# Optimization experiments

Measured on AMD Instinct MI355X. Metric: run time of the kernel, lower is better.

## Reference

```python
import jax, jax.numpy as jnp
import numpy as np

SEQ, SUB, B, V = 32, 16, 512, 258
U = SEQ // SUB
Z, CH, CO, DH = 512, 1024, 512, 1024


def _lstm_cell(x, h, c, Wi, Wh, bi, bh):
    # torch gate order: input, forget, cell, output
    g = x @ Wi + h @ Wh + bi + bh  # [B, 4H]
    i, f, gg, o = jnp.split(g, 4, axis=-1)
    c = jax.nn.sigmoid(f) * c + jax.nn.sigmoid(i) * jnp.tanh(gg)
    h = jax.nn.sigmoid(o) * jnp.tanh(c)
    return h, c


def _lstm2(xs, h1_0, p1, p2):
    # xs: [T,B,in]; h1_0: [B,H] layer-1 initial hidden.
    # Layer-2 hidden and both cell states start at zero (initialize_state in torch code).
    z0 = jnp.zeros_like(h1_0)
    def step(carry, x):
        h1, c1, h2, c2 = carry
        h1, c1 = _lstm_cell(x, h1, c1, *p1)
        h2, c2 = _lstm_cell(h1, h2, c2, *p2)
        return (h1, c1, h2, c2), h2
    _, hs = jax.lax.scan(step, (h1_0, z0, z0, z0), xs)
    return hs  # [T,B,H] top-layer hidden states


def setup_inputs() -> dict:
    key = jax.random.key(0)
    ks = iter(jax.random.split(key, 40))
    def w(shape, s=0.05):
        return jax.random.normal(next(ks), shape, dtype=jnp.float32) * s
    return {
        "z": jax.random.normal(next(ks), (B, Z), dtype=jnp.float32),
        "x": jax.random.uniform(next(ks), (SEQ, B, V), dtype=jnp.float32),
        "conductor_input": w((1, B, V)),
        "ci_W": w((Z, CH)), "ci_b": w((CH,)),
        "cW1i": w((V, 4 * CH)), "cW1h": w((CH, 4 * CH)), "cb1i": w((4 * CH,)), "cb1h": w((4 * CH,)),
        "cW2i": w((CH, 4 * CH)), "cW2h": w((CH, 4 * CH)), "cb2i": w((4 * CH,)), "cb2h": w((4 * CH,)),
        "co_W": w((CH, CO)), "co_b": w((CO,)),
        "di_W": w((CO, DH)), "di_b": w((DH,)),
        "dW1i": w((CO + V, 4 * DH)), "dW1h": w((DH, 4 * DH)), "db1i": w((4 * DH,)), "db1h": w((4 * DH,)),
        "dW2i": w((DH, 4 * DH)), "dW2h": w((DH, 4 * DH)), "db2i": w((4 * DH,)), "db2h": w((4 * DH,)),
        "fc_W": w((DH, V)), "fc_b": w((V,)),
    }


def reference(z, x, conductor_input, ci_W, ci_b, cW1i, cW1h, cb1i, cb1h, cW2i, cW2h, cb2i, cb2h, co_W, co_b, di_W, di_b, dW1i, dW1h, db1i, db1h, dW2i, dW2h, db2i, db2h, fc_W, fc_b):
    # --- conductor: 2-layer LSTM over U steps of a learned constant input ---
    h1 = jnp.tanh(z @ ci_W + ci_b)  # [B,CH] layer-1 init hidden
    cin = jnp.broadcast_to(conductor_input, (U, B, V))
    ch = _lstm2(cin, h1, (cW1i, cW1h, cb1i, cb1h), (cW2i, cW2h, cb2i, cb2h))  # [U,B,CH]
    c = ch @ co_W + co_b  # [U,B,CO]
    # --- decoder (teacher forcing): state resets each sub-sequence, so the U
    # segments of length SUB are independent given c -> vmap over segments ---
    sos = jnp.zeros((1, B, V), jnp.float32).at[:, :, 0].set(1.0)
    prev = jnp.concatenate([sos, x[:-1]], axis=0).reshape(U, SUB, B, V)
    cb = jnp.broadcast_to(c[:, None], (U, SUB, B, CO))
    dec_in = jnp.concatenate([cb, prev], axis=-1)  # [U,SUB,B,CO+V]
    def run_seg(xs, cj):
        h1_0 = jnp.tanh(cj @ di_W + di_b)  # [B,DH]
        return _lstm2(xs, h1_0, (dW1i, dW1h, db1i, db1h), (dW2i, dW2h, db2i, db2h))
    hs = jax.vmap(run_seg)(dec_in, c)  # [U,SUB,B,DH]
    logp = jax.nn.log_softmax(hs @ fc_W + fc_b, axis=-1)  # log(softmax(.)) fused
    return logp.reshape(SEQ, B, V).transpose(1, 0, 2)  # [B,SEQ,V]
```

## Files before the change

kernel.cpp:

```cpp
#include <hip/hip_runtime.h>
#include <cstddef>
#include <cstdint>


namespace {

typedef short s8v __attribute__((ext_vector_type(8)));
typedef float f4v __attribute__((ext_vector_type(4)));
typedef unsigned short ushort_t;

__device__ inline unsigned short f2bf(float f) {
    union { float f; unsigned u; } v; v.f = f;
    unsigned r = v.u + 0x7fff + ((v.u >> 16) & 1);
    return (unsigned short)(r >> 16);
}
__device__ inline float bf2f(ushort_t u) {
    union { unsigned u; float f; } v; v.u = ((unsigned)u) << 16; return v.f;
}
__device__ inline float sigm_f(float x) { return 1.f / (1.f + __expf(-x)); }
__device__ inline float tanh_f(float x) {
    const float e = __expf(2.f * fabsf(x));
    return copysignf(1.f - 2.f / (e + 1.f), x);
}

#define GLOAD_LDS(gp, lp)                                              \
    __builtin_amdgcn_global_load_lds(                                  \
        (const __attribute__((address_space(1))) void*)(gp),           \
        (__attribute__((address_space(3))) void*)(lp), 16, 0, 0)

__device__ __forceinline__ void gemm_core(
    const ushort_t* __restrict__ A1a, const ushort_t* __restrict__ A1b,
    int lda1, int K1, const ushort_t* __restrict__ B1t,
    const ushort_t* __restrict__ A2, int lda2, int K2,
    const ushort_t* __restrict__ B2t,
    int bm, int bn, ushort_t* lds, f4v acc[4][4])
{
    const int tid = threadIdx.x;
    const int wid = tid >> 6;
    const int lane = tid & 63;

    const int sr0 = wid * 16 + (lane >> 2);
    const int sr1 = sr0 + 64;
    const int rl0 = sr0 ^ ((sr0 >> 2) & 1);
    const int rl1 = sr1 ^ ((sr1 >> 2) & 1);
    const int c0 = (((lane & 3) ^ (rl0 & 3)) << 3);
    const int c1 = (((lane & 3) ^ (rl1 & 3)) << 3);
    const int ldst = wid * 512;

    auto arow = [&](const ushort_t* Aa, const ushort_t* Ab, int lda,
                    int r) -> const ushort_t* {
        return (Ab != nullptr && r >= 512) ? Ab + (size_t)(r - 512) * lda
                                           : Aa + (size_t)r * lda;
    };
    const ushort_t* a1r0 = arow(A1a, A1b, lda1, bm + rl0) + c0;
    const ushort_t* a1r1 = arow(A1a, A1b, lda1, bm + rl1) + c1;
    const ushort_t* b1r0 = B1t + (size_t)(bn + rl0) * K1 + c0;
    const ushort_t* b1r1 = B1t + (size_t)(bn + rl1) * K1 + c1;
    const int n1 = K1 >> 5, n2 = (B2t != nullptr) ? (K2 >> 5) : 0;
    const int nt = n1 + n2;
    const ushort_t* a2r0 = nullptr; const ushort_t* a2r1 = nullptr;
    const ushort_t* b2r0 = nullptr; const ushort_t* b2r1 = nullptr;
    if (n2 > 0) {
        a2r0 = A2 + (size_t)(bm + rl0) * lda2 + c0;
        a2r1 = A2 + (size_t)(bm + rl1) * lda2 + c1;
        b2r0 = B2t + (size_t)(bn + rl0) * K2 + c0;
        b2r1 = B2t + (size_t)(bn + rl1) * K2 + c1;
    }

    auto stage = [&](int idx, int buf) {
        ushort_t* Lb = lds + buf * 8192;
        const ushort_t *pa0, *pa1, *pb0, *pb1;
        if (idx < n1) {
            const int k0 = idx << 5;
            pa0 = a1r0 + k0; pa1 = a1r1 + k0; pb0 = b1r0 + k0; pb1 = b1r1 + k0;
        } else {
            const int k0 = (idx - n1) << 5;
            pa0 = a2r0 + k0; pa1 = a2r1 + k0; pb0 = b2r0 + k0; pb1 = b2r1 + k0;
        }
        GLOAD_LDS(pa0, Lb + ldst);
        GLOAD_LDS(pa1, Lb + 2048 + ldst);
        GLOAD_LDS(pb0, Lb + 4096 + ldst);
        GLOAD_LDS(pb1, Lb + 6144 + ldst);
    };

    const int wr = wid >> 1, wc = wid & 1;
    const int lrow = lane & 15, lkg = lane >> 4;
    int aoff[4], boff[4];
#pragma unroll
    for (int m = 0; m < 4; ++m) {
        const int r = wr * 64 + m * 16 + lrow;
        aoff[m] = (r ^ ((r >> 2) & 1)) * 32 + ((lkg ^ (r & 3)) << 3);
    }
#pragma unroll
    for (int n = 0; n < 4; ++n) {
        const int r = wc * 64 + n * 16 + lrow;
        boff[n] = 4096 + (r ^ ((r >> 2) & 1)) * 32 + ((lkg ^ (r & 3)) << 3);
    }

    stage(0, 0);
    stage(1, 1);
    int sbuf = 2, cbuf = 0;
    for (int t = 0; t < nt; ++t) {
        if (t == nt - 1) {
            asm volatile("s_waitcnt vmcnt(0)" ::: "memory");
        } else {
            asm volatile("s_waitcnt vmcnt(4)" ::: "memory");
        }
        __builtin_amdgcn_s_barrier();
        __builtin_amdgcn_sched_barrier(0);
        if (t + 2 < nt) {
            stage(t + 2, sbuf);
            sbuf = (sbuf == 2) ? 0 : sbuf + 1;
        }
        const ushort_t* L = lds + cbuf * 8192;
        s8v af[4], bv[4];
#pragma unroll
        for (int m = 0; m < 4; ++m) af[m] = *(const s8v*)(L + aoff[m]);
#pragma unroll
        for (int n = 0; n < 4; ++n) bv[n] = *(const s8v*)(L + boff[n]);
        __builtin_amdgcn_s_setprio(1);
#pragma unroll
        for (int m = 0; m < 4; ++m)
#pragma unroll
            for (int n = 0; n < 4; ++n)
                acc[m][n] = __builtin_amdgcn_mfma_f32_16x16x32_bf16(
                    af[m], bv[n], acc[m][n], 0, 0, 0);
        __builtin_amdgcn_s_setprio(0);
        cbuf = (cbuf == 2) ? 0 : cbuf + 1;
    }
}

template <int ACT>
__global__ __launch_bounds__(256) void plain_gemm(
    const ushort_t* __restrict__ A, int lda, int K,
    const ushort_t* __restrict__ Bt,
    const float* __restrict__ bias, int bias_n,
    float* __restrict__ C, ushort_t* __restrict__ Cbf, int N)
{
    __shared__ __align__(16) ushort_t lds[3 * 8192];
    const int bm = blockIdx.x * 128, bn = blockIdx.y * 128;
    f4v acc[4][4] = {};
    gemm_core(A, nullptr, lda, K, Bt, nullptr, 0, 0, nullptr, bm, bn, lds, acc);

    const int tid = threadIdx.x, wid = tid >> 6, lane = tid & 63;
    const int wr = wid >> 1, wc = wid & 1, lrow = lane & 15, lkg = lane >> 4;
#pragma unroll
    for (int m = 0; m < 4; ++m) {
        const int row0 = bm + wr * 64 + m * 16 + lkg * 4;
#pragma unroll
        for (int n = 0; n < 4; ++n) {
            const int col = bn + wc * 64 + n * 16 + lrow;
            const float bv = (bias != nullptr && col < bias_n) ? bias[col] : 0.f;
#pragma unroll
            for (int r = 0; r < 4; ++r) {
                float v = acc[m][n][r] + bv;
                if (ACT == 1) v = tanh_f(v);
                const size_t o = (size_t)(row0 + r) * N + col;
                if (C != nullptr) C[o] = v;
                if (Cbf != nullptr) Cbf[o] = f2bf(v);
            }
        }
    }
}

struct Prob {
    const ushort_t* A1a; const ushort_t* A1b; int lda1; int K1;
    const ushort_t* B1t;
    const ushort_t* A2; int lda2; int K2; const ushort_t* B2t;
    const ushort_t* Dbf;
    const float* bias;
    float* cst;
    ushort_t* hout;
    ushort_t* hs;
    int step_s;
};

__global__ __launch_bounds__(256) void lstm_step(Prob PA, int nxa, Prob PB,
                                                 int mshift)
{
    __shared__ __align__(16) ushort_t lds[3 * 8192];
    const int nblk = gridDim.x;
    const int wg = blockIdx.x;
    const int swz = (wg & 7) * (nblk >> 3) + (wg >> 3);
    const int nmb = 1 << mshift;
    const int nb = swz >> mshift;
    const int mb = swz & (nmb - 1);

    const bool isA = mb < nxa;
    const Prob& P = isA ? PA : PB;
    const int bm = (isA ? mb : mb - nxa) * 128;
    const int bn = nb * 128;

    f4v acc[4][4] = {};
    gemm_core(P.A1a, P.A1b, P.lda1, P.K1, P.B1t,
              P.A2, P.lda2, P.K2, P.B2t, bm, bn, lds, acc);

    const int tid = threadIdx.x, wid = tid >> 6, lane = tid & 63;
    const int wr = wid >> 1, wc = wid & 1, lrow = lane & 15, lkg = lane >> 4;
    const int colbase = bn + wc * 64;
    const int jb = (colbase >> 6) * 16 + lrow;

#pragma unroll
    for (int m = 0; m < 4; ++m) {
        const int row0 = bm + wr * 64 + m * 16 + lkg * 4;
#pragma unroll
        for (int r = 0; r < 4; ++r) {
            const int row = row0 + r;
            float g0 = acc[m][0][r], g1 = acc[m][1][r];
            float g2 = acc[m][2][r], g3 = acc[m][3][r];
            if (P.Dbf != nullptr) {
                const ushort_t* d = P.Dbf + (size_t)row * 4096 + colbase + lrow;
                g0 += bf2f(d[0]); g1 += bf2f(d[16]);
                g2 += bf2f(d[32]); g3 += bf2f(d[48]);
            }
            if (P.bias != nullptr) {
                const float* b = P.bias + colbase + lrow;
                g0 += b[0]; g1 += b[16]; g2 += b[32]; g3 += b[48];
            }
            const size_t ci = (size_t)row * 1024 + jb;
            const float cn = fmaf(sigm_f(g1), P.cst[ci], sigm_f(g0) * tanh_f(g2));
            const float hn = sigm_f(g3) * tanh_f(cn);
            P.cst[ci] = cn;
            const ushort_t hb = f2bf(hn);
            P.hout[ci] = hb;
            if (P.hs != nullptr) {
                size_t d;
                if (P.step_s >= 0) {
                    const int u = row >> 9, b = row & 511;
                    d = ((size_t)((u * 16 + P.step_s) * 512 + b) << 10) + jb;
                } else {
                    d = ci;
                }
                P.hs[d] = hb;
            }
        }
    }
}

template <int PERM>
__global__ __launch_bounds__(256) void transpose_to_bf16(
    const float* __restrict__ in, ushort_t* __restrict__ out,
    int K, int N, int Kp, int Np)
{
    __shared__ float tile[32][33];
    const int k0 = blockIdx.x * 32, n0 = blockIdx.y * 32;
    const int tx = threadIdx.x, ty = threadIdx.y;
#pragma unroll
    for (int q = 0; q < 4; ++q) {
        const int k = k0 + ty + 8 * q, n = n0 + tx;
        tile[ty + 8 * q][tx] = (k < K && n < N) ? in[(size_t)k * N + n] : 0.f;
    }
    __syncthreads();
#pragma unroll
    for (int q = 0; q < 4; ++q) {
        const int n = n0 + ty + 8 * q, k = k0 + tx;
        int np = n;
        if (PERM) np = ((n & 1023) >> 4) * 64 + (n >> 10) * 16 + (n & 15);
        out[(size_t)np * Kp + k] = f2bf(tile[tx][ty + 8 * q]);
    }
}

__global__ void convert_pad_bf16(const float* __restrict__ in,
                                 ushort_t* __restrict__ out,
                                 int K, int Kp, int total)
{
    const int idx = blockIdx.x * 256 + threadIdx.x;
    if (idx >= total) return;
    const int r = idx / Kp, k = idx - r * Kp;
    out[idx] = (k < K) ? f2bf(in[(size_t)r * K + k]) : (ushort_t)0;
}

__global__ void sos_init_bf16(ushort_t* __restrict__ sos)
{
    const int i = blockIdx.x * 256 + threadIdx.x;
    if (i < 512 * 288) sos[i] = ((i % 288) == 0) ? (ushort_t)0x3F80 : (ushort_t)0;
}

__global__ void permute_bias(const float* __restrict__ b1,
                             const float* __restrict__ b2,
                             float* __restrict__ out)
{
    const int c = blockIdx.x * 256 + threadIdx.x;
    if (c >= 4096) return;
    const int g = (c >> 4) & 3;
    const int j = (c >> 6) * 16 + (c & 15);
    out[c] = b1[g * 1024 + j] + b2[g * 1024 + j];
}

__global__ __launch_bounds__(256) void logsoftmax_kernel(
    const float* __restrict__ logits, float* __restrict__ out)
{
    const int row = blockIdx.x;
    const int tid = threadIdx.x;
    const float* L = logits + (size_t)row * 384;
    const int t = row >> 9;
    const int b = row & 511;
    float* O = out + ((size_t)b * 32 + t) * 258;

    const float x0 = L[tid];
    const float x1 = (tid < 2) ? L[256 + tid] : -1e30f;

    __shared__ float sm[4];
    float m = fmaxf(x0, x1);
#pragma unroll
    for (int off = 32; off > 0; off >>= 1) m = fmaxf(m, __shfl_down(m, off));
    if ((tid & 63) == 0) sm[tid >> 6] = m;
    __syncthreads();
    m = fmaxf(fmaxf(sm[0], sm[1]), fmaxf(sm[2], sm[3]));
    __syncthreads();

    float s = expf(x0 - m) + ((tid < 2) ? expf(x1 - m) : 0.f);
#pragma unroll
    for (int off = 32; off > 0; off >>= 1) s += __shfl_down(s, off);
    if ((tid & 63) == 0) sm[tid >> 6] = s;
    __syncthreads();
    s = sm[0] + sm[1] + sm[2] + sm[3];

    const float lse = m + logf(s);
    O[tid] = x0 - lse;
    if (tid < 2) O[256 + tid] = x1 - lse;
}

}

extern "C" void kernel_launch(void* const* d_in, const int* in_sizes, int n_in,
                              void* d_out, int out_size, void* d_ws, size_t ws_size,
                              hipStream_t stream)
{
    (void)in_sizes; (void)n_in; (void)out_size; (void)ws_size;

    const float* z    = (const float*)d_in[0];
    const float* x    = (const float*)d_in[1];
    const float* cin  = (const float*)d_in[2];
    const float* ciW  = (const float*)d_in[3];
    const float* cib  = (const float*)d_in[4];
    const float* cW1i = (const float*)d_in[5];
    const float* cW1h = (const float*)d_in[6];
    const float* cb1i = (const float*)d_in[7];
    const float* cb1h = (const float*)d_in[8];
    const float* cW2i = (const float*)d_in[9];
    const float* cW2h = (const float*)d_in[10];
    const float* cb2i = (const float*)d_in[11];
    const float* cb2h = (const float*)d_in[12];
    const float* coW  = (const float*)d_in[13];
    const float* cob  = (const float*)d_in[14];
    const float* diW  = (const float*)d_in[15];
    const float* dib  = (const float*)d_in[16];
    const float* dW1i = (const float*)d_in[17];
    const float* dW1h = (const float*)d_in[18];
    const float* db1i = (const float*)d_in[19];
    const float* db1h = (const float*)d_in[20];
    const float* dW2i = (const float*)d_in[21];
    const float* dW2h = (const float*)d_in[22];
    const float* db2i = (const float*)d_in[23];
    const float* db2h = (const float*)d_in[24];
    const float* fcW  = (const float*)d_in[25];
    const float* fcb  = (const float*)d_in[26];
    float* out = (float*)d_out;

    char* wsp = (char*)d_ws;
    size_t off = 0;
    auto allocf = [&](size_t n) { float* p = (float*)(wsp + off); off += n * 4; return p; };
    auto allocb = [&](size_t n) { ushort_t* p = (ushort_t*)(wsp + off); off += n * 2; return p; };

    float* cst = allocf((size_t)3 * 1024 * 1024 + 64);
    float* c1c = cst;
    float* c2c = cst + (size_t)512 * 1024;
    float* c1d = cst + (size_t)1024 * 1024;
    float* c2d = cst + (size_t)2 * 1024 * 1024;
    float* pb1c = allocf(4096);
    float* pb2c = allocf(4096);
    float* pb1d = allocf(4096);
    float* pb2d = allocf(4096);
    float* logits = allocf((size_t)16384 * 384);

    ushort_t* h2z  = allocb((size_t)2 * (512 + 1024) * 1024);
    ushort_t* hc2A = h2z;
    ushort_t* hc2B = h2z + (size_t)512 * 1024;
    ushort_t* h2dA = h2z + (size_t)2 * 512 * 1024;
    ushort_t* h2dB = h2z + (size_t)(2 * 512 + 1024) * 1024;

    ushort_t* hc1A = allocb((size_t)512 * 1024);
    ushort_t* hc1B = allocb((size_t)512 * 1024);
    ushort_t* h1dA = allocb((size_t)1024 * 1024);
    ushort_t* h1dB = allocb((size_t)1024 * 1024);

    ushort_t* zbf    = allocb((size_t)512 * 512);
    ushort_t* cinbf  = allocb((size_t)512 * 288);
    ushort_t* sosbf  = allocb((size_t)512 * 288);
    ushort_t* xbf    = allocb((size_t)16384 * 288);
    ushort_t* chbf   = allocb((size_t)1024 * 1024);
    ushort_t* ccode  = allocb((size_t)1024 * 512);
    ushort_t* cpre   = allocb((size_t)1024 * 4096);
    ushort_t* xW1c   = allocb((size_t)512 * 4096);
    ushort_t* hsbf   = allocb((size_t)16384 * 1024);

    ushort_t* ciWt  = allocb((size_t)1024 * 512);
    ushort_t* cW1it = allocb((size_t)4096 * 288);
    ushort_t* cW1ht = allocb((size_t)4096 * 1024);
    ushort_t* cW2it = allocb((size_t)4096 * 1024);
    ushort_t* cW2ht = allocb((size_t)4096 * 1024);
    ushort_t* coWt  = allocb((size_t)512 * 1024);
    ushort_t* dtopt = allocb((size_t)4096 * 512);
    ushort_t* dbott = allocb((size_t)4096 * 288);
    ushort_t* diWt  = allocb((size_t)1024 * 512);
    ushort_t* dW1ht = allocb((size_t)4096 * 1024);
    ushort_t* dW2it = allocb((size_t)4096 * 1024);
    ushort_t* dW2ht = allocb((size_t)4096 * 1024);
    ushort_t* fcWt  = allocb((size_t)384 * 1024);

    hipMemsetAsync(cst, 0, (size_t)3 * 1024 * 1024 * 4, stream);
    hipMemsetAsync(h2z, 0, (size_t)2 * (512 + 1024) * 1024 * 2, stream);

    auto transp = [&](const float* in, ushort_t* o, int K, int N, int Kp, int Np, int perm) {
        dim3 g(Kp / 32, Np / 32), b(32, 8);
        if (perm) transpose_to_bf16<1><<<g, b, 0, stream>>>(in, o, K, N, Kp, Np);
        else      transpose_to_bf16<0><<<g, b, 0, stream>>>(in, o, K, N, Kp, Np);
    };
    transp(ciW, ciWt, 512, 1024, 512, 1024, 0);
    transp(cW1i, cW1it, 258, 4096, 288, 4096, 1);
    transp(cW1h, cW1ht, 1024, 4096, 1024, 4096, 1);
    transp(cW2i, cW2it, 1024, 4096, 1024, 4096, 1);
    transp(cW2h, cW2ht, 1024, 4096, 1024, 4096, 1);
    transp(coW, coWt, 1024, 512, 1024, 512, 0);
    transp(dW1i, dtopt, 512, 4096, 512, 4096, 1);
    transp(dW1i + (size_t)512 * 4096, dbott, 258, 4096, 288, 4096, 1);
    transp(diW, diWt, 512, 1024, 512, 1024, 0);
    transp(dW1h, dW1ht, 1024, 4096, 1024, 4096, 1);
    transp(dW2i, dW2it, 1024, 4096, 1024, 4096, 1);
    transp(dW2h, dW2ht, 1024, 4096, 1024, 4096, 1);
    transp(fcW, fcWt, 1024, 258, 1024, 384, 0);

    auto convert = [&](const float* in, ushort_t* o, int K, int Kp, int R) {
        const int total = R * Kp;
        convert_pad_bf16<<<dim3((total + 255) / 256), 256, 0, stream>>>(in, o, K, Kp, total);
    };
    convert(z, zbf, 512, 512, 512);
    convert(cin, cinbf, 258, 288, 512);
    convert(x, xbf, 258, 288, 16384);
    sos_init_bf16<<<dim3((512 * 288 + 255) / 256), 256, 0, stream>>>(sosbf);
    permute_bias<<<16, 256, 0, stream>>>(cb1i, cb1h, pb1c);
    permute_bias<<<16, 256, 0, stream>>>(cb2i, cb2h, pb2c);
    permute_bias<<<16, 256, 0, stream>>>(db1i, db1h, pb1d);
    permute_bias<<<16, 256, 0, stream>>>(db2i, db2h, pb2d);

    auto gemm = [&](int act, const ushort_t* A, int lda, int K, const ushort_t* Bt,
                    const float* bias, int bias_n,
                    float* C, ushort_t* Cbf, int M, int N) {
        dim3 g(M / 128, N / 128);
        if (act) plain_gemm<1><<<g, 256, 0, stream>>>(A, lda, K, Bt, bias, bias_n, C, Cbf, N);
        else     plain_gemm<0><<<g, 256, 0, stream>>>(A, lda, K, Bt, bias, bias_n, C, Cbf, N);
    };

    gemm(1, zbf, 512, 512, ciWt, cib, 1024, nullptr, hc1A, 512, 1024);
    gemm(0, cinbf, 288, 288, cW1it, pb1c, 4096, nullptr, xW1c, 512, 4096);

    ushort_t* HC1[2] = {hc1A, hc1B};
    ushort_t* HC2[2] = {hc2A, hc2B};
    for (int k = 0; k <= 2; ++k) {
        Prob pa{}, pb{};
        int nxa = 0, nxb = 0;
        if (k < 2) {
            pa = {HC1[k & 1], nullptr, 1024, 1024, cW1ht,
                  nullptr, 0, 0, nullptr,
                  xW1c, nullptr, c1c, HC1[(k + 1) & 1], nullptr, -1};
            nxa = 4;
        }
        if (k >= 1) {
            pb = {HC1[k & 1], nullptr, 1024, 1024, cW2it,
                  HC2[k & 1], 1024, 1024, cW2ht,
                  nullptr, pb2c, c2c, HC2[(k + 1) & 1],
                  chbf + (size_t)(k - 1) * 512 * 1024, -1};
            nxb = 4;
        }
        const int nmb = nxa + nxb;
        const int mshift = (nmb == 4) ? 2 : 3;
        lstm_step<<<dim3(nmb * 32), 256, 0, stream>>>(pa, nxa, pb, mshift);
    }

    gemm(0, chbf, 1024, 1024, coWt, cob, 512, nullptr, ccode, 1024, 512);
    gemm(0, ccode, 512, 512, dtopt, pb1d, 4096, nullptr, cpre, 1024, 4096);
    gemm(1, ccode, 512, 512, diWt, dib, 1024, nullptr, h1dA, 1024, 1024);

    ushort_t* H1[2] = {h1dA, h1dB};
    ushort_t* H2[2] = {h2dA, h2dB};
    for (int k = 0; k <= 16; ++k) {
        Prob pa{}, pb{};
        int nxa = 0, nxb = 0;
        if (k < 16) {
            const ushort_t* plo = (k == 0) ? sosbf : (xbf + (size_t)(k - 1) * 512 * 288);
            const ushort_t* phi = xbf + (size_t)(15 + k) * 512 * 288;
            pa = {plo, phi, 288, 288, dbott,
                  H1[k & 1], 1024, 1024, dW1ht,
                  cpre, nullptr, c1d, H1[(k + 1) & 1], nullptr, -1};
            nxa = 8;
        }
        if (k >= 1) {
            pb = {H1[k & 1], nullptr, 1024, 1024, dW2it,
                  H2[k & 1], 1024, 1024, dW2ht,
                  nullptr, pb2d, c2d, H2[(k + 1) & 1], hsbf, k - 1};
            nxb = 8;
        }
        const int nmb = nxa + nxb;
        const int mshift = (nmb == 8) ? 3 : 4;
        lstm_step<<<dim3(nmb * 32), 256, 0, stream>>>(pa, nxa, pb, mshift);
    }

    gemm(0, hsbf, 1024, 1024, fcWt, fcb, 258, logits, nullptr, 16384, 384);
    logsoftmax_kernel<<<dim3(16384), 256, 0, stream>>>(logits, out);
}
```

Baseline: 1.108 ms.

## Pre-pack weights into MFMA fragment layout and load B directly to registers

```diff
diff --git a/kernel.cpp b/kernel.cpp
--- a/kernel.cpp
+++ b/kernel.cpp
@@ -30,117 +30,118 @@
 
 __device__ __forceinline__ void gemm_core(
     const ushort_t* __restrict__ A1a, const ushort_t* __restrict__ A1b,
-    int lda1, int K1, const ushort_t* __restrict__ B1t,
+    int lda1, int K1, const ushort_t* __restrict__ W1,
     const ushort_t* __restrict__ A2, int lda2, int K2,
-    const ushort_t* __restrict__ B2t,
+    const ushort_t* __restrict__ W2,
     int bm, int bn, ushort_t* lds, f4v acc[4][4])
 {
     const int tid = threadIdx.x;
     const int wid = tid >> 6;
     const int lane = tid & 63;
-
-    const int sr0 = wid * 16 + (lane >> 2);
-    const int sr1 = sr0 + 64;
-    const int rl0 = sr0 ^ ((sr0 >> 2) & 1);
-    const int rl1 = sr1 ^ ((sr1 >> 2) & 1);
-    const int c0 = (((lane & 3) ^ (rl0 & 3)) << 3);
-    const int c1 = (((lane & 3) ^ (rl1 & 3)) << 3);
-    const int ldst = wid * 512;
+    const int wr = wid >> 1, wc = wid & 1;
+    const int lrow = lane & 15, lkg = lane >> 4;
+
+    const int n1 = K1 >> 5;
+    const int n2 = (W2 != nullptr) ? (K2 >> 5) : 0;
+    const int nt = n1 + n2;
+
+    const int row0 = wid * 16 + (lane >> 2);
+    const int row1 = row0 + 64;
+    const int src0 = (((lane & 3) ^ ((row0 >> 1) & 3)) << 3);
+    const int src1 = (((lane & 3) ^ ((row1 >> 1) & 3)) << 3);
 
     auto arow = [&](const ushort_t* Aa, const ushort_t* Ab, int lda,
                     int r) -> const ushort_t* {
         return (Ab != nullptr && r >= 512) ? Ab + (size_t)(r - 512) * lda
                                            : Aa + (size_t)r * lda;
     };
-    const ushort_t* a1r0 = arow(A1a, A1b, lda1, bm + rl0) + c0;
-    const ushort_t* a1r1 = arow(A1a, A1b, lda1, bm + rl1) + c1;
-    const ushort_t* b1r0 = B1t + (size_t)(bn + rl0) * K1 + c0;
-    const ushort_t* b1r1 = B1t + (size_t)(bn + rl1) * K1 + c1;
-    const int n1 = K1 >> 5, n2 = (B2t != nullptr) ? (K2 >> 5) : 0;
-    const int nt = n1 + n2;
-    const ushort_t* a2r0 = nullptr; const ushort_t* a2r1 = nullptr;
-    const ushort_t* b2r0 = nullptr; const ushort_t* b2r1 = nullptr;
+    const ushort_t* pA1q0 = arow(A1a, A1b, lda1, bm + row0) + src0;
+    const ushort_t* pA1q1 = arow(A1a, A1b, lda1, bm + row1) + src1;
+    const ushort_t* pA2q0 = nullptr;
+    const ushort_t* pA2q1 = nullptr;
     if (n2 > 0) {
-        a2r0 = A2 + (size_t)(bm + rl0) * lda2 + c0;
-        a2r1 = A2 + (size_t)(bm + rl1) * lda2 + c1;
-        b2r0 = B2t + (size_t)(bn + rl0) * K2 + c0;
-        b2r1 = B2t + (size_t)(bn + rl1) * K2 + c1;
-    }
-
-    auto stage = [&](int idx, int buf) {
-        ushort_t* Lb = lds + buf * 8192;
-        const ushort_t *pa0, *pa1, *pb0, *pb1;
-        if (idx < n1) {
-            const int k0 = idx << 5;
-            pa0 = a1r0 + k0; pa1 = a1r1 + k0; pb0 = b1r0 + k0; pb1 = b1r1 + k0;
-        } else {
-            const int k0 = (idx - n1) << 5;
-            pa0 = a2r0 + k0; pa1 = a2r1 + k0; pb0 = b2r0 + k0; pb1 = b2r1 + k0;
-        }
-        GLOAD_LDS(pa0, Lb + ldst);
-        GLOAD_LDS(pa1, Lb + 2048 + ldst);
-        GLOAD_LDS(pb0, Lb + 4096 + ldst);
-        GLOAD_LDS(pb1, Lb + 6144 + ldst);
-    };
-
-    const int wr = wid >> 1, wc = wid & 1;
-    const int lrow = lane & 15, lkg = lane >> 4;
-    int aoff[4], boff[4];
+        pA2q0 = A2 + (size_t)(bm + row0) * lda2 + src0;
+        pA2q1 = A2 + (size_t)(bm + row1) * lda2 + src1;
+    }
+
+    int sbuf = 2;
+    auto stageA = [&](int idx, int buf) {
+        const ushort_t *p0, *p1;
+        if (idx < n1) { p0 = pA1q0 + (idx << 5); p1 = pA1q1 + (idx << 5); }
+        else { const int i2 = idx - n1; p0 = pA2q0 + (i2 << 5); p1 = pA2q1 + (i2 << 5); }
+        GLOAD_LDS(p0, lds + buf * 4096 + wid * 512);
+        GLOAD_LDS(p1, lds + buf * 4096 + 2048 + wid * 512);
+    };
+
+    const int nb0 = (bn >> 4) + wc * 4;
+    const ushort_t* W1l = W1 + (size_t)nb0 * n1 * 512 + lane * 8;
+    const ushort_t* W2l = (n2 > 0) ? (W2 + (size_t)nb0 * n2 * 512 + lane * 8) : nullptr;
+
+    auto loadB = [&](int t, s8v (&b)[4]) {
+        const ushort_t* base; int kb, KB;
+        if (t < n1) { base = W1l; kb = t; KB = n1; }
+        else        { base = W2l; kb = t - n1; KB = n2; }
+#pragma unroll
+        for (int n = 0; n < 4; ++n)
+            b[n] = *(const s8v*)(base + ((size_t)(n * KB + kb) << 9));
+    };
+
+    int aoff[4];
 #pragma unroll
     for (int m = 0; m < 4; ++m) {
         const int r = wr * 64 + m * 16 + lrow;
-        aoff[m] = (r ^ ((r >> 2) & 1)) * 32 + ((lkg ^ (r & 3)) << 3);
-    }
-#pragma unroll
-    for (int n = 0; n < 4; ++n) {
-        const int r = wc * 64 + n * 16 + lrow;
-        boff[n] = 4096 + (r ^ ((r >> 2) & 1)) * 32 + ((lkg ^ (r & 3)) << 3);
-    }
-
-    stage(0, 0);
-    stage(1, 1);
-    int sbuf = 2, cbuf = 0;
-    for (int t = 0; t < nt; ++t) {
-        if (t == nt - 1) {
-            asm volatile("s_waitcnt vmcnt(0)" ::: "memory");
-        } else {
-            asm volatile("s_waitcnt vmcnt(4)" ::: "memory");
-        }
+        aoff[m] = r * 32 + ((lkg ^ ((r >> 1) & 3)) << 3);
+    }
+
+    s8v bA[4], bB[4];
+    loadB(0, bA);
+    stageA(0, 0);
+    if (nt > 1) stageA(1, 1);
+
+    int cbuf = 0;
+    auto iter = [&](int t, s8v (&bcur)[4], s8v (&bnxt)[4]) {
+        if (t + 1 < nt) loadB(t + 1, bnxt);
+        if (t + 1 < nt) asm volatile("s_waitcnt vmcnt(6)" ::: "memory");
+        else            asm volatile("s_waitcnt vmcnt(0)" ::: "memory");
         __builtin_amdgcn_s_barrier();
         __builtin_amdgcn_sched_barrier(0);
         if (t + 2 < nt) {
-            stage(t + 2, sbuf);
+            stageA(t + 2, sbuf);
             sbuf = (sbuf == 2) ? 0 : sbuf + 1;
         }
-        const ushort_t* L = lds + cbuf * 8192;
-        s8v af[4], bv[4];
-#pragma unroll
-        for (int m = 0; m < 4; ++m) af[m] = *(const s8v*)(L + aoff[m]);
-#pragma unroll
-        for (int n = 0; n < 4; ++n) bv[n] = *(const s8v*)(L + boff[n]);
+        const ushort_t* L = lds + cbuf * 4096;
+        s8v a[4];
+#pragma unroll
+        for (int m = 0; m < 4; ++m) a[m] = *(const s8v*)(L + aoff[m]);
         __builtin_amdgcn_s_setprio(1);
 #pragma unroll
         for (int m = 0; m < 4; ++m)
 #pragma unroll
             for (int n = 0; n < 4; ++n)
                 acc[m][n] = __builtin_amdgcn_mfma_f32_16x16x32_bf16(
-                    af[m], bv[n], acc[m][n], 0, 0, 0);
+                    a[m], bcur[n], acc[m][n], 0, 0, 0);
         __builtin_amdgcn_s_setprio(0);
         cbuf = (cbuf == 2) ? 0 : cbuf + 1;
+    };
+
+    int t = 0;
+    while (true) {
+        iter(t, bA, bB); if (++t == nt) break;
+        iter(t, bB, bA); if (++t == nt) break;
     }
 }
 
 template <int ACT>
-__global__ __launch_bounds__(256) void plain_gemm(
+__global__ __launch_bounds__(256, 2) void plain_gemm(
     const ushort_t* __restrict__ A, int lda, int K,
-    const ushort_t* __restrict__ Bt,
+    const ushort_t* __restrict__ W,
     const float* __restrict__ bias, int bias_n,
     float* __restrict__ C, ushort_t* __restrict__ Cbf, int N)
 {
-    __shared__ __align__(16) ushort_t lds[3 * 8192];
+    __shared__ __align__(16) ushort_t lds[3 * 4096];
     const int bm = blockIdx.x * 128, bn = blockIdx.y * 128;
     f4v acc[4][4] = {};
-    gemm_core(A, nullptr, lda, K, Bt, nullptr, 0, 0, nullptr, bm, bn, lds, acc);
+    gemm_core(A, nullptr, lda, K, W, nullptr, 0, 0, nullptr, bm, bn, lds, acc);
 
     const int tid = threadIdx.x, wid = tid >> 6, lane = tid & 63;
     const int wr = wid >> 1, wc = wid & 1, lrow = lane & 15, lkg = lane >> 4;
@@ -175,10 +176,10 @@
     int step_s;
 };
 
-__global__ __launch_bounds__(256) void lstm_step(Prob PA, int nxa, Prob PB,
-                                                 int mshift)
-{
-    __shared__ __align__(16) ushort_t lds[3 * 8192];
+__global__ __launch_bounds__(256, 2) void lstm_step(Prob PA, int nxa, Prob PB,
+                                                    int mshift)
+{
+    __shared__ __align__(16) ushort_t lds[3 * 4096];
     const int nblk = gridDim.x;
     const int wg = blockIdx.x;
     const int swz = (wg & 7) * (nblk >> 3) + (wg >> 3);
@@ -238,26 +239,39 @@
 }
 
 template <int PERM>
-__global__ __launch_bounds__(256) void transpose_to_bf16(
+__global__ __launch_bounds__(256) void pack_frag_bf16(
     const float* __restrict__ in, ushort_t* __restrict__ out,
     int K, int N, int Kp, int Np)
 {
     __shared__ float tile[32][33];
-    const int k0 = blockIdx.x * 32, n0 = blockIdx.y * 32;
-    const int tx = threadIdx.x, ty = threadIdx.y;
+    const int kb = blockIdx.x;
+    const int np0 = blockIdx.y * 32;
+    const int k0 = kb * 32;
+    const int tx = threadIdx.x & 31;
+    const int ty = threadIdx.x >> 5;
 #pragma unroll
     for (int q = 0; q < 4; ++q) {
-        const int k = k0 + ty + 8 * q, n = n0 + tx;
+        const int k = k0 + ty + 8 * q;
+        const int np = np0 + tx;
+        int n;
+        if (PERM) n = ((np >> 4) & 3) * 1024 + (np >> 6) * 16 + (np & 15);
+        else      n = np;
         tile[ty + 8 * q][tx] = (k < K && n < N) ? in[(size_t)k * N + n] : 0.f;
     }
     __syncthreads();
-#pragma unroll
-    for (int q = 0; q < 4; ++q) {
-        const int n = n0 + ty + 8 * q, k = k0 + tx;
-        int np = n;
-        if (PERM) np = ((n & 1023) >> 4) * 64 + (n >> 10) * 16 + (n & 15);
-        out[(size_t)np * Kp + k] = f2bf(tile[tx][ty + 8 * q]);
-    }
+    const int t = threadIdx.x;
+    const int rec = t >> 7;
+    const int lane = (t >> 1) & 63;
+    const int half = t & 1;
+    const size_t grec = (size_t)(np0 / 16 + rec) * (Kp / 32) + kb;
+    const int kl = (lane >> 4) * 8 + half * 4;
+    const int nl = rec * 16 + (lane & 15);
+    ushort4 v;
+    v.x = f2bf(tile[kl + 0][nl]);
+    v.y = f2bf(tile[kl + 1][nl]);
+    v.z = f2bf(tile[kl + 2][nl]);
+    v.w = f2bf(tile[kl + 3][nl]);
+    *(ushort4*)(out + (grec * 64 + lane) * 8 + half * 4) = v;
 }
 
 __global__ void convert_pad_bf16(const float* __restrict__ in,
@@ -273,7 +287,7 @@
 __global__ void sos_init_bf16(ushort_t* __restrict__ sos)
 {
     const int i = blockIdx.x * 256 + threadIdx.x;
-    if (i < 512 * 288) sos[i] = ((i % 288) == 0) ? (ushort_t)0x3F80 : (ushort_t)0;
+    if (i < 512 * 320) sos[i] = ((i % 320) == 0) ? (ushort_t)0x3F80 : (ushort_t)0;
 }
 
 __global__ void permute_bias(const float* __restrict__ b1,
@@ -386,74 +400,74 @@
     ushort_t* h1dB = allocb((size_t)1024 * 1024);
 
     ushort_t* zbf    = allocb((size_t)512 * 512);
-    ushort_t* cinbf  = allocb((size_t)512 * 288);
-    ushort_t* sosbf  = allocb((size_t)512 * 288);
-    ushort_t* xbf    = allocb((size_t)16384 * 288);
+    ushort_t* cinbf  = allocb((size_t)512 * 320);
+    ushort_t* sosbf  = allocb((size_t)512 * 320);
+    ushort_t* xbf    = allocb((size_t)16384 * 320);
     ushort_t* chbf   = allocb((size_t)1024 * 1024);
     ushort_t* ccode  = allocb((size_t)1024 * 512);
     ushort_t* cpre   = allocb((size_t)1024 * 4096);
     ushort_t* xW1c   = allocb((size_t)512 * 4096);
     ushort_t* hsbf   = allocb((size_t)16384 * 1024);
 
-    ushort_t* ciWt  = allocb((size_t)1024 * 512);
-    ushort_t* cW1it = allocb((size_t)4096 * 288);
-    ushort_t* cW1ht = allocb((size_t)4096 * 1024);
-    ushort_t* cW2it = allocb((size_t)4096 * 1024);
-    ushort_t* cW2ht = allocb((size_t)4096 * 1024);
-    ushort_t* coWt  = allocb((size_t)512 * 1024);
-    ushort_t* dtopt = allocb((size_t)4096 * 512);
-    ushort_t* dbott = allocb((size_t)4096 * 288);
-    ushort_t* diWt  = allocb((size_t)1024 * 512);
-    ushort_t* dW1ht = allocb((size_t)4096 * 1024);
-    ushort_t* dW2it = allocb((size_t)4096 * 1024);
-    ushort_t* dW2ht = allocb((size_t)4096 * 1024);
-    ushort_t* fcWt  = allocb((size_t)384 * 1024);
+    ushort_t* ciWp  = allocb((size_t)1024 * 512);
+    ushort_t* cW1ip = allocb((size_t)4096 * 320);
+    ushort_t* cW1hp = allocb((size_t)4096 * 1024);
+    ushort_t* cW2ip = allocb((size_t)4096 * 1024);
+    ushort_t* cW2hp = allocb((size_t)4096 * 1024);
+    ushort_t* coWp  = allocb((size_t)512 * 1024);
+    ushort_t* dtopp = allocb((size_t)4096 * 512);
+    ushort_t* dbotp = allocb((size_t)4096 * 320);
+    ushort_t* diWp  = allocb((size_t)1024 * 512);
+    ushort_t* dW1hp = allocb((size_t)4096 * 1024);
+    ushort_t* dW2ip = allocb((size_t)4096 * 1024);
+    ushort_t* dW2hp = allocb((size_t)4096 * 1024);
+    ushort_t* fcWp  = allocb((size_t)384 * 1024);
 
     hipMemsetAsync(cst, 0, (size_t)3 * 1024 * 1024 * 4, stream);
     hipMemsetAsync(h2z, 0, (size_t)2 * (512 + 1024) * 1024 * 2, stream);
 
-    auto transp = [&](const float* in, ushort_t* o, int K, int N, int Kp, int Np, int perm) {
-        dim3 g(Kp / 32, Np / 32), b(32, 8);
-        if (perm) transpose_to_bf16<1><<<g, b, 0, stream>>>(in, o, K, N, Kp, Np);
-        else      transpose_to_bf16<0><<<g, b, 0, stream>>>(in, o, K, N, Kp, Np);
-    };
-    transp(ciW, ciWt, 512, 1024, 512, 1024, 0);
-    transp(cW1i, cW1it, 258, 4096, 288, 4096, 1);
-    transp(cW1h, cW1ht, 1024, 4096, 1024, 4096, 1);
-    transp(cW2i, cW2it, 1024, 4096, 1024, 4096, 1);
-    transp(cW2h, cW2ht, 1024, 4096, 1024, 4096, 1);
-    transp(coW, coWt, 1024, 512, 1024, 512, 0);
-    transp(dW1i, dtopt, 512, 4096, 512, 4096, 1);
-    transp(dW1i + (size_t)512 * 4096, dbott, 258, 4096, 288, 4096, 1);
-    transp(diW, diWt, 512, 1024, 512, 1024, 0);
-    transp(dW1h, dW1ht, 1024, 4096, 1024, 4096, 1);
-    transp(dW2i, dW2it, 1024, 4096, 1024, 4096, 1);
-    transp(dW2h, dW2ht, 1024, 4096, 1024, 4096, 1);
-    transp(fcW, fcWt, 1024, 258, 1024, 384, 0);
+    auto pack = [&](const float* in, ushort_t* o, int K, int N, int Kp, int Np, int perm) {
+        dim3 g(Kp / 32, Np / 32);
+        if (perm) pack_frag_bf16<1><<<g, 256, 0, stream>>>(in, o, K, N, Kp, Np);
+        else      pack_frag_bf16<0><<<g, 256, 0, stream>>>(in, o, K, N, Kp, Np);
+    };
+    pack(ciW, ciWp, 512, 1024, 512, 1024, 0);
+    pack(cW1i, cW1ip, 258, 4096, 320, 4096, 1);
+    pack(cW1h, cW1hp, 1024, 4096, 1024, 4096, 1);
+    pack(cW2i, cW2ip, 1024, 4096, 1024, 4096, 1);
+    pack(cW2h, cW2hp, 1024, 4096, 1024, 4096, 1);
+    pack(coW, coWp, 1024, 512, 1024, 512, 0);
+    pack(dW1i, dtopp, 512, 4096, 512, 4096, 1);
+    pack(dW1i + (size_t)512 * 4096, dbotp, 258, 4096, 320, 4096, 1);
+    pack(diW, diWp, 512, 1024, 512, 1024, 0);
+    pack(dW1h, dW1hp, 1024, 4096, 1024, 4096, 1);
+    pack(dW2i, dW2ip, 1024, 4096, 1024, 4096, 1);
+    pack(dW2h, dW2hp, 1024, 4096, 1024, 4096, 1);
+    pack(fcW, fcWp, 1024, 258, 1024, 384, 0);
 
     auto convert = [&](const float* in, ushort_t* o, int K, int Kp, int R) {
         const int total = R * Kp;
         convert_pad_bf16<<<dim3((total + 255) / 256), 256, 0, stream>>>(in, o, K, Kp, total);
     };
     convert(z, zbf, 512, 512, 512);
-    convert(cin, cinbf, 258, 288, 512);
-    convert(x, xbf, 258, 288, 16384);
-    sos_init_bf16<<<dim3((512 * 288 + 255) / 256), 256, 0, stream>>>(sosbf);
+    convert(cin, cinbf, 258, 320, 512);
+    convert(x, xbf, 258, 320, 16384);
+    sos_init_bf16<<<dim3((512 * 320 + 255) / 256), 256, 0, stream>>>(sosbf);
     permute_bias<<<16, 256, 0, stream>>>(cb1i, cb1h, pb1c);
     permute_bias<<<16, 256, 0, stream>>>(cb2i, cb2h, pb2c);
     permute_bias<<<16, 256, 0, stream>>>(db1i, db1h, pb1d);
     permute_bias<<<16, 256, 0, stream>>>(db2i, db2h, pb2d);
 
-    auto gemm = [&](int act, const ushort_t* A, int lda, int K, const ushort_t* Bt,
+    auto gemm = [&](int act, const ushort_t* A, int lda, int K, const ushort_t* W,
                     const float* bias, int bias_n,
                     float* C, ushort_t* Cbf, int M, int N) {
         dim3 g(M / 128, N / 128);
-        if (act) plain_gemm<1><<<g, 256, 0, stream>>>(A, lda, K, Bt, bias, bias_n, C, Cbf, N);
-        else     plain_gemm<0><<<g, 256, 0, stream>>>(A, lda, K, Bt, bias, bias_n, C, Cbf, N);
-    };
-
-    gemm(1, zbf, 512, 512, ciWt, cib, 1024, nullptr, hc1A, 512, 1024);
-    gemm(0, cinbf, 288, 288, cW1it, pb1c, 4096, nullptr, xW1c, 512, 4096);
+        if (act) plain_gemm<1><<<g, 256, 0, stream>>>(A, lda, K, W, bias, bias_n, C, Cbf, N);
+        else     plain_gemm<0><<<g, 256, 0, stream>>>(A, lda, K, W, bias, bias_n, C, Cbf, N);
+    };
+
+    gemm(1, zbf, 512, 512, ciWp, cib, 1024, nullptr, hc1A, 512, 1024);
+    gemm(0, cinbf, 320, 320, cW1ip, pb1c, 4096, nullptr, xW1c, 512, 4096);
 
     ushort_t* HC1[2] = {hc1A, hc1B};
     ushort_t* HC2[2] = {hc2A, hc2B};
@@ -461,14 +475,14 @@
         Prob pa{}, pb{};
         int nxa = 0, nxb = 0;
         if (k < 2) {
-            pa = {HC1[k & 1], nullptr, 1024, 1024, cW1ht,
+            pa = {HC1[k & 1], nullptr, 1024, 1024, cW1hp,
                   nullptr, 0, 0, nullptr,
                   xW1c, nullptr, c1c, HC1[(k + 1) & 1], nullptr, -1};
             nxa = 4;
         }
         if (k >= 1) {
-            pb = {HC1[k & 1], nullptr, 1024, 1024, cW2it,
-                  HC2[k & 1], 1024, 1024, cW2ht,
+            pb = {HC1[k & 1], nullptr, 1024, 1024, cW2ip,
+                  HC2[k & 1], 1024, 1024, cW2hp,
                   nullptr, pb2c, c2c, HC2[(k + 1) & 1],
                   chbf + (size_t)(k - 1) * 512 * 1024, -1};
             nxb = 4;
@@ -478,9 +492,9 @@
         lstm_step<<<dim3(nmb * 32), 256, 0, stream>>>(pa, nxa, pb, mshift);
     }
 
-    gemm(0, chbf, 1024, 1024, coWt, cob, 512, nullptr, ccode, 1024, 512);
-    gemm(0, ccode, 512, 512, dtopt, pb1d, 4096, nullptr, cpre, 1024, 4096);
-    gemm(1, ccode, 512, 512, diWt, dib, 1024, nullptr, h1dA, 1024, 1024);
+    gemm(0, chbf, 1024, 1024, coWp, cob, 512, nullptr, ccode, 1024, 512);
+    gemm(0, ccode, 512, 512, dtopp, pb1d, 4096, nullptr, cpre, 1024, 4096);
+    gemm(1, ccode, 512, 512, diWp, dib, 1024, nullptr, h1dA, 1024, 1024);
 
     ushort_t* H1[2] = {h1dA, h1dB};
     ushort_t* H2[2] = {h2dA, h2dB};
@@ -488,16 +502,16 @@
         Prob pa{}, pb{};
         int nxa = 0, nxb = 0;
         if (k < 16) {
-            const ushort_t* plo = (k == 0) ? sosbf : (xbf + (size_t)(k - 1) * 512 * 288);
-            const ushort_t* phi = xbf + (size_t)(15 + k) * 512 * 288;
-            pa = {plo, phi, 288, 288, dbott,
-                  H1[k & 1], 1024, 1024, dW1ht,
+            const ushort_t* plo = (k == 0) ? sosbf : (xbf + (size_t)(k - 1) * 512 * 320);
+            const ushort_t* phi = xbf + (size_t)(15 + k) * 512 * 320;
+            pa = {plo, phi, 320, 320, dbotp,
+                  H1[k & 1], 1024, 1024, dW1hp,
                   cpre, nullptr, c1d, H1[(k + 1) & 1], nullptr, -1};
             nxa = 8;
         }
         if (k >= 1) {
-            pb = {H1[k & 1], nullptr, 1024, 1024, dW2it,
-                  H2[k & 1], 1024, 1024, dW2ht,
+            pb = {H1[k & 1], nullptr, 1024, 1024, dW2ip,
+                  H2[k & 1], 1024, 1024, dW2hp,
                   nullptr, pb2d, c2d, H2[(k + 1) & 1], hsbf, k - 1};
             nxb = 8;
         }
@@ -506,6 +520,6 @@
         lstm_step<<<dim3(nmb * 32), 256, 0, stream>>>(pa, nxa, pb, mshift);
     }
 
-    gemm(0, hsbf, 1024, 1024, fcWt, fcb, 258, logits, nullptr, 16384, 384);
+    gemm(0, hsbf, 1024, 1024, fcWp, fcb, 258, logits, nullptr, 16384, 384);
     logsoftmax_kernel<<<dim3(16384), 256, 0, stream>>>(logits, out);
 }
```

Result: slower. 1.193 ms (+7.6%).
